# Kernel optimization log

Hardware: AMD Instinct MI355X
Metric: run time of the kernel (lower is better)

## Reference

```python
import math
import jax, jax.numpy as jnp
import numpy as np

B, N, T, H = 4, 64, 384, 256
LAGS = (1, 5, 21)
L = len(LAGS)
NU = 500  # peer-universe size for rank buffers
TOPK = 8
LN_EPS = 1e-5


def setup_inputs() -> dict:
    key = jax.random.key(0)
    ks = jax.random.split(key, 24)
    s = 1.0 / np.sqrt(H)

    def lin(i):
        w = jax.random.uniform(ks[i], (H, H), jnp.float32, -s, s)
        b = jax.random.uniform(ks[i + 1], (H,), jnp.float32, -s, s)
        return w, b

    wq_w, wq_b = lin(0)
    wk_w, wk_b = lin(2)
    wv_w, wv_b = lin(4)
    f1_w, f1_b = lin(6)
    f2_w, f2_b = lin(8)
    return dict(
        target_h=jax.random.normal(ks[10], (B, T, H), jnp.float32),
        peer_h=jax.random.normal(ks[11], (B, N, T, H), jnp.float32),
        wq_w=wq_w, wq_b=wq_b, wk_w=wk_w, wk_b=wk_b, wv_w=wv_w, wv_b=wv_b,
        f1_w=f1_w, f1_b=f1_b, f2_w=f2_w, f2_b=f2_b,
        ln_g=jnp.ones((H,), jnp.float32),
        ln_b=jnp.zeros((H,), jnp.float32),
        alpha=jnp.float32(0.1),
        log_rank_strength=jnp.log(jnp.clip(jax.random.uniform(ks[12], (L, NU, NU)), 1e-6, None)),
        peer_mask=jnp.ones((B, N), dtype=bool),
        rank_topk_mask=jax.random.uniform(ks[13], (L, NU, NU)) < 0.2,
        target_id=jax.random.randint(ks[14], (B,), 0, NU),
        peer_id=jax.random.randint(ks[15], (B, N), 0, NU),
    )


def _forward(target_h, peer_h, wq_w, wq_b, wk_w, wk_b, wv_w, wv_b,
             f1_w, f1_b, f2_w, f2_b, ln_g, ln_b, alpha, log_rank_strength,
             peer_mask, rank_topk_mask, target_id, peer_id):
    lags = jnp.array(LAGS, dtype=jnp.int32)
    t_idx = jnp.arange(T, dtype=jnp.int32)[None, :] - lags[:, None]   # [L,T]
    valid_time = t_idx >= 0                                           # [L,T]
    t_idx_c = jnp.maximum(t_idx, 0)

    # lag-gathered peer features: [B,N,L,T,H] -> [B,T,N,L,H]
    peer_h_lag = jnp.transpose(peer_h[:, :, t_idx_c, :], (0, 3, 1, 2, 4))

    Q = target_h @ wq_w.T + wq_b                  # [B,T,H]
    K = peer_h_lag @ wk_w.T + wk_b                # [B,T,N,L,H]
    # delta-valued V path (use_delta_value=True): current minus lagged
    peer_h_now = jnp.transpose(peer_h, (0, 2, 1, 3))[:, :, :, None, :]  # [B,T,N,1,H]
    V = (peer_h_now - peer_h_lag) @ wv_w.T + wv_b  # [B,T,N,L,H]

    logits = jnp.einsum('bth,btnlh->btnl', Q, K) / math.sqrt(H)  # [B,T,N,L]

    # Bennett soft bias (use_bennett=True)
    tgt_b = jnp.broadcast_to(target_id[:, None], (B, N))          # [B,N]
    prior = jnp.transpose(log_rank_strength[:, peer_id, tgt_b], (1, 2, 0))  # [B,N,L]
    logits = logits + alpha * prior[:, None, :, :]

    neg_inf = jnp.float32(-jnp.inf)
    logits = jnp.where(valid_time.T[None, :, None, :], logits, neg_inf)      # time validity
    logits = jnp.where(peer_mask[:, None, :, None], logits, neg_inf)         # peer mask
    rmask = jnp.transpose(rank_topk_mask[:, peer_id, tgt_b], (1, 2, 0))      # [B,N,L]
    logits = jnp.where(rmask[:, None, :, :], logits, neg_inf)                # hard rank mask

    NL = N * L
    k = min(TOPK, NL)
    logits_flat = logits.reshape(B, T, NL)
    topk_vals, topk_idx = jax.lax.top_k(logits_flat, k)            # [B,T,k]
    is_inf = jnp.isinf(topk_vals)
    all_inf = jnp.all(is_inf, axis=-1, keepdims=True)
    topk_safe = jnp.where(is_inf, jnp.float32(-1e9), topk_vals)
    weights = jax.nn.softmax(topk_safe, axis=-1)
    weights = weights * (~all_inf).astype(weights.dtype)

    V_flat = V.reshape(B, T, NL, H)
    V_sel = jnp.take_along_axis(V_flat, topk_idx[..., None], axis=2)  # [B,T,k,H]
    ll_y = jnp.sum(weights[..., None] * V_sel, axis=2)                # [B,T,H]

    ffn = jax.nn.elu(ll_y @ f1_w.T + f1_b) @ f2_w.T + f2_b
    x = ll_y + ffn
    mu = jnp.mean(x, axis=-1, keepdims=True)
    var = jnp.var(x, axis=-1, keepdims=True)
    return (x - mu) / jnp.sqrt(var + LN_EPS) * ln_g + ln_b


def reference(target_h, peer_h, wq_w, wq_b, wk_w, wk_b, wv_w, wv_b,
              f1_w, f1_b, f2_w, f2_b, ln_g, ln_b, alpha, log_rank_strength,
              peer_mask, rank_topk_mask, target_id, peer_id):
    return _forward(target_h, peer_h, wq_w, wq_b, wk_w, wk_b, wv_w, wv_b,
                    f1_w, f1_b, f2_w, f2_b, ln_g, ln_b, alpha, log_rank_strength,
                    peer_mask, rank_topk_mask, target_id, peer_id)
```

## Files before the change

### kernel.cpp

```cpp
#include <hip/hip_runtime.h>
#include <hip/hip_bf16.h>

typedef unsigned short u16;

#define NU_ 500

__device__ __forceinline__ float b2f(u16 u){
  union { unsigned int i; float f; } v; v.i = ((unsigned int)u) << 16; return v.f;
}
__device__ __forceinline__ void up2(unsigned int u, float& a, float& b){
  a = b2f((u16)(u & 0xffffu)); b = b2f((u16)(u >> 16));
}

template<typename FT> __device__ __forceinline__ float ldf(const FT* p, long i);
template<> __device__ __forceinline__ float ldf<float>(const float* p, long i){ return p[i]; }
template<> __device__ __forceinline__ float ldf<u16>(const u16* p, long i){ return b2f(p[i]); }

template<typename FT> __device__ __forceinline__ float4 ld4(const FT* p);
template<> __device__ __forceinline__ float4 ld4<float>(const float* p){ return *(const float4*)p; }
template<> __device__ __forceinline__ float4 ld4<u16>(const u16* p){
  uint2 u = *(const uint2*)p; float4 r; up2(u.x, r.x, r.y); up2(u.y, r.z, r.w); return r;
}

template<typename FT> __device__ __forceinline__ void ld8(const FT* p, float* o);
template<> __device__ __forceinline__ void ld8<float>(const float* p, float* o){
  float4 a = ((const float4*)p)[0], b = ((const float4*)p)[1];
  o[0]=a.x; o[1]=a.y; o[2]=a.z; o[3]=a.w; o[4]=b.x; o[5]=b.y; o[6]=b.z; o[7]=b.w;
}
template<> __device__ __forceinline__ void ld8<u16>(const u16* p, float* o){
  uint4 u = ((const uint4*)p)[0];
  up2(u.x,o[0],o[1]); up2(u.y,o[2],o[3]); up2(u.z,o[4],o[5]); up2(u.w,o[6],o[7]);
}

template<typename FT> __device__ __forceinline__ void stf(void* p, long i, float v);
template<> __device__ __forceinline__ void stf<float>(void* p, long i, float v){ ((float*)p)[i] = v; }
template<> __device__ __forceinline__ void stf<u16>(void* p, long i, float v){
  ((__hip_bfloat16*)p)[i] = __float2bfloat16(v);
}

__device__ __forceinline__ bool mask_at(const void* p, long i, int mode){
  if (mode == 1) return ((const unsigned char*)p)[i] != 0;
  if (mode == 2) return ((const u16*)p)[i] != 0;
  return ((const unsigned int*)p)[i] != 0;
}

__global__ void detect_kernel(const u16* __restrict__ lng,
                              const unsigned char* __restrict__ pm,
                              int* __restrict__ flags){
  if (threadIdx.x == 0){
    flags[0] = (lng[0] == 0x3F80u) ? 1 : 0;
    const unsigned char p0 = pm[0], p1 = pm[1];
    int m;
    if (p0 == 0x01u)      m = (p1 == 0x01u) ? 1 : 0;
    else if (p0 == 0x80u) m = 2;
    else                  m = 0;
    flags[1] = m;
  }
}

template<typename FT>
__global__ __launch_bounds__(256) void qproj_kernel(
    const FT* __restrict__ xg, const FT* __restrict__ wq, const FT* __restrict__ wqb,
    const FT* __restrict__ wk, const FT* __restrict__ wkb,
    float* __restrict__ Qt, float* __restrict__ qb, const int* __restrict__ flags, int me)
{
  if (flags[0] != me) return;
  __shared__ __align__(16) float xs[8][256];
  __shared__ __align__(16) float qs[8][256];
  const int j = threadIdx.x;
  const int row0 = blockIdx.x * 8;
  #pragma unroll
  for (int r = 0; r < 8; ++r) xs[r][j] = ldf<FT>(xg, (long)(row0 + r) * 256 + j);
  __syncthreads();

  float acc[8];
  #pragma unroll
  for (int r = 0; r < 8; ++r) acc[r] = 0.f;
  for (int h8 = 0; h8 < 32; ++h8){
    float w[8]; ld8<FT>(wq + (long)j * 256 + h8 * 8, w);
    const int h = h8 * 8;
    #pragma unroll
    for (int r = 0; r < 8; ++r){
      const float* xr = &xs[r][h];
      acc[r] += xr[0]*w[0] + xr[1]*w[1] + xr[2]*w[2] + xr[3]*w[3]
              + xr[4]*w[4] + xr[5]*w[5] + xr[6]*w[6] + xr[7]*w[7];
    }
  }
  const float bq = ldf<FT>(wqb, j);
  #pragma unroll
  for (int r = 0; r < 8; ++r) qs[r][j] = acc[r] + bq;
  __syncthreads();

  float at[8];
  #pragma unroll
  for (int r = 0; r < 8; ++r) at[r] = 0.f;
  for (int h = 0; h < 256; ++h){
    const float w = ldf<FT>(wk, (long)h * 256 + j);
    #pragma unroll
    for (int r = 0; r < 8; ++r) at[r] += qs[r][h] * w;
  }
  #pragma unroll
  for (int r = 0; r < 8; ++r) Qt[(long)(row0 + r) * 256 + j] = at[r];

  const float bk = ldf<FT>(wkb, j);
  #pragma unroll
  for (int r = 0; r < 8; ++r) xs[r][j] = qs[r][j] * bk;
  __syncthreads();
  if (j < 8){
    float s = 0.f;
    for (int h = 0; h < 256; ++h) s += xs[j][h];
    qb[row0 + j] = s;
  }
}

template<typename FT>
__global__ __launch_bounds__(256) void attn_kernel(
    const FT* __restrict__ peer_h, const float* __restrict__ Qt, const float* __restrict__ qbv,
    const FT* __restrict__ lrs, const void* __restrict__ pmask, const void* __restrict__ rmask,
    const int* __restrict__ target_id, const int* __restrict__ peer_id,
    const FT* __restrict__ alpha_p, const int* __restrict__ flags,
    float* __restrict__ dvec, float* __restrict__ ssum, int me)
{
  if (flags[0] != me) return;
  __shared__ __align__(16) float qt_s[256];
  __shared__ float lg[192];
  __shared__ int   seli[8];
  __shared__ float selw[8];
  __shared__ int   allinf_sh;
  const int bt = blockIdx.x;
  const int b = bt / 384, t = bt % 384;
  const int tid = threadIdx.x;
  const int lane = tid & 63, wv = tid >> 6;
  const float NEG_INF = -__builtin_inff();

  qt_s[tid] = Qt[(long)bt * 256 + tid];
  __syncthreads();
  const float qb    = qbv[bt];
  const float alpha = ldf<FT>(alpha_p, 0);
  const int   tgt   = target_id[b];
  const int   mmode = flags[1];
  const int   lags[3] = {1, 5, 21};

  const float4 qv = *(const float4*)&qt_s[lane * 4];

  for (int c = wv; c < 192; c += 4){
    const int n = c / 3, l = c - n * 3;
    const int lag = lags[l];
    const int pid = peer_id[b * 64 + n];
    const long ridx = (long)l * (NU_*NU_) + (long)pid * NU_ + tgt;
    bool ok = (t >= lag);
    if (ok) ok = mask_at(pmask, b * 64 + n, mmode) && mask_at(rmask, ridx, mmode);
    float logit = NEG_INF;
    if (ok){
      const int tc = t - lag;
      const FT* rp = peer_h + (((long)(b*64 + n)) * 384 + tc) * 256;
      float4 a = ld4<FT>(rp + lane * 4);
      float p = a.x*qv.x + a.y*qv.y + a.z*qv.z + a.w*qv.w;
      #pragma unroll
      for (int off = 32; off; off >>= 1) p += __shfl_xor(p, off);
      logit = (p + qb) * 0.0625f + alpha * ldf<FT>(lrs, ridx);
    }
    if (lane == 0) lg[c] = logit;
  }
  __syncthreads();

  if (wv == 0){
    float v0 = lg[lane], v1 = lg[lane + 64], v2 = lg[lane + 128];
    float sv[8]; int si[8];
    for (int k = 0; k < 8; ++k){
      float mv = v0; int mi = lane;
      if (v1 > mv){ mv = v1; mi = lane + 64; }
      if (v2 > mv){ mv = v2; mi = lane + 128; }
      #pragma unroll
      for (int off = 32; off; off >>= 1){
        float ov = __shfl_xor(mv, off);
        int   oi = __shfl_xor(mi, off);
        if (ov > mv || (ov == mv && oi < mi)){ mv = ov; mi = oi; }
      }
      sv[k] = mv; si[k] = mi;
      if      (mi == lane)       v0 = NEG_INF;
      else if (mi == lane + 64)  v1 = NEG_INF;
      else if (mi == lane + 128) v2 = NEG_INF;
    }
    const int allinf = (sv[0] == NEG_INF) ? 1 : 0;
    const float m = allinf ? -1e9f : sv[0];
    float e[8]; float tot = 0.f;
    #pragma unroll
    for (int k = 0; k < 8; ++k){
      const float s = (sv[k] == NEG_INF) ? -1e9f : sv[k];
      e[k] = expf(s - m);
      tot += e[k];
    }
    if (lane == 0){
      allinf_sh = allinf;
      const float inv = 1.f / tot;
      for (int k = 0; k < 8; ++k){
        seli[k] = si[k];
        selw[k] = allinf ? 0.f : e[k] * inv;
      }
    }
  }
  __syncthreads();

  float acc = 0.f;
  const int h = tid;
  #pragma unroll
  for (int k = 0; k < 8; ++k){
    const float w = selw[k];
    if (w != 0.f){
      const int c = seli[k];
      const int n = c / 3, l = c - n * 3;
      const int tc = t - lags[l];
      const long base = ((long)(b*64 + n)) * 384;
      acc += w * (ldf<FT>(peer_h, (base + t ) * 256 + h)
                - ldf<FT>(peer_h, (base + tc) * 256 + h));
    }
  }
  dvec[(long)bt * 256 + h] = acc;
  if (tid == 0) ssum[bt] = allinf_sh ? 0.f : 1.f;
}

template<typename FT>
__global__ __launch_bounds__(256) void ffn_kernel(
    const float* __restrict__ dv, const float* __restrict__ sv,
    const FT* __restrict__ wv, const FT* __restrict__ wvb,
    const FT* __restrict__ f1, const FT* __restrict__ f1b,
    const FT* __restrict__ f2, const FT* __restrict__ f2b,
    const FT* __restrict__ lng, const FT* __restrict__ lnb,
    void* __restrict__ out, const int* __restrict__ flags, int me)
{
  if (flags[0] != me) return;
  __shared__ __align__(16) float ds[8][256];
  __shared__ __align__(16) float ys[8][256];
  __shared__ float mu_s[8], rs_s[8];
  const int j = threadIdx.x;
  const int row0 = blockIdx.x * 8;
  #pragma unroll
  for (int r = 0; r < 8; ++r) ds[r][j] = dv[(long)(row0 + r) * 256 + j];
  __syncthreads();

  float ll[8];
  {
    #pragma unroll
    for (int r = 0; r < 8; ++r) ll[r] = 0.f;
    for (int h8 = 0; h8 < 32; ++h8){
      float w[8]; ld8<FT>(wv + (long)j * 256 + h8 * 8, w);
      const int h = h8 * 8;
      #pragma unroll
      for (int r = 0; r < 8; ++r){
        const float* xr = &ds[r][h];
        ll[r] += xr[0]*w[0] + xr[1]*w[1] + xr[2]*w[2] + xr[3]*w[3]
               + xr[4]*w[4] + xr[5]*w[5] + xr[6]*w[6] + xr[7]*w[7];
      }
    }
    const float bv = ldf<FT>(wvb, j);
    #pragma unroll
    for (int r = 0; r < 8; ++r) ll[r] += sv[row0 + r] * bv;
  }
  #pragma unroll
  for (int r = 0; r < 8; ++r) ys[r][j] = ll[r];
  __syncthreads();

  {
    float a[8];
    #pragma unroll
    for (int r = 0; r < 8; ++r) a[r] = 0.f;
    for (int h8 = 0; h8 < 32; ++h8){
      float w[8]; ld8<FT>(f1 + (long)j * 256 + h8 * 8, w);
      const int h = h8 * 8;
      #pragma unroll
      for (int r = 0; r < 8; ++r){
        const float* xr = &ys[r][h];
        a[r] += xr[0]*w[0] + xr[1]*w[1] + xr[2]*w[2] + xr[3]*w[3]
              + xr[4]*w[4] + xr[5]*w[5] + xr[6]*w[6] + xr[7]*w[7];
      }
    }
    const float b1 = ldf<FT>(f1b, j);
    #pragma unroll
    for (int r = 0; r < 8; ++r){
      const float x = a[r] + b1;
      ds[r][j] = (x > 0.f) ? x : expm1f(x);
    }
  }
  __syncthreads();

  float xv[8];
  {
    float a[8];
    #pragma unroll
    for (int r = 0; r < 8; ++r) a[r] = 0.f;
    for (int h8 = 0; h8 < 32; ++h8){
      float w[8]; ld8<FT>(f2 + (long)j * 256 + h8 * 8, w);
      const int h = h8 * 8;
      #pragma unroll
      for (int r = 0; r < 8; ++r){
        const float* xr = &ds[r][h];
        a[r] += xr[0]*w[0] + xr[1]*w[1] + xr[2]*w[2] + xr[3]*w[3]
              + xr[4]*w[4] + xr[5]*w[5] + xr[6]*w[6] + xr[7]*w[7];
      }
    }
    const float b2_ = ldf<FT>(f2b, j);
    #pragma unroll
    for (int r = 0; r < 8; ++r) xv[r] = ll[r] + a[r] + b2_;
  }
  #pragma unroll
  for (int r = 0; r < 8; ++r) ys[r][j] = xv[r];
  __syncthreads();

  {
    const int lane = j & 63, wvi = j >> 6;
    for (int rr = 0; rr < 2; ++rr){
      const int r = wvi * 2 + rr;
      float s = 0.f, q = 0.f;
      for (int p = lane; p < 256; p += 64){ const float x = ys[r][p]; s += x; q += x * x; }
      #pragma unroll
      for (int off = 32; off; off >>= 1){ s += __shfl_xor(s, off); q += __shfl_xor(q, off); }
      if (lane == 0){
        const float mu = s * (1.f/256.f);
        const float var = q * (1.f/256.f) - mu * mu;
        mu_s[r] = mu; rs_s[r] = rsqrtf(var + 1e-5f);
      }
    }
  }
  __syncthreads();
  const float gj = ldf<FT>(lng, j), bj = ldf<FT>(lnb, j);
  #pragma unroll
  for (int r = 0; r < 8; ++r){
    const float o = (ys[r][j] - mu_s[r]) * rs_s[r] * gj + bj;
    stf<FT>(out, (long)(row0 + r) * 256 + j, o);
  }
}

extern "C" void kernel_launch(void* const* d_in, const int* in_sizes, int n_in,
                              void* d_out, int out_size, void* d_ws, size_t ws_size,
                              hipStream_t stream)
{
  (void)in_sizes; (void)n_in; (void)out_size; (void)ws_size;
  const void* target_h = d_in[0];
  const void* peer_h   = d_in[1];
  const void* wq_w = d_in[2];  const void* wq_b = d_in[3];
  const void* wk_w = d_in[4];  const void* wk_b = d_in[5];
  const void* wv_w = d_in[6];  const void* wv_b = d_in[7];
  const void* f1_w = d_in[8];  const void* f1_b = d_in[9];
  const void* f2_w = d_in[10]; const void* f2_b = d_in[11];
  const void* ln_g = d_in[12]; const void* ln_b = d_in[13];
  const void* alpha = d_in[14];
  const void* lrs  = d_in[15];
  const void* pmask = d_in[16];
  const void* rmask = d_in[17];
  const int* target_id = (const int*)d_in[18];
  const int* peer_id   = (const int*)d_in[19];

  int*   flags = (int*)d_ws;
  float* Qt    = (float*)d_ws + 16;
  float* qb    = Qt + 393216;
  float* dvec  = qb + 1536;
  float* ssum  = dvec + 393216;

  detect_kernel<<<1, 64, 0, stream>>>((const u16*)ln_g, (const unsigned char*)pmask, flags);

  qproj_kernel<float><<<192, 256, 0, stream>>>((const float*)target_h, (const float*)wq_w,
      (const float*)wq_b, (const float*)wk_w, (const float*)wk_b, Qt, qb, flags, 0);
  attn_kernel<float><<<1536, 256, 0, stream>>>((const float*)peer_h, Qt, qb,
      (const float*)lrs, pmask, rmask, target_id, peer_id, (const float*)alpha,
      flags, dvec, ssum, 0);
  ffn_kernel<float><<<192, 256, 0, stream>>>(dvec, ssum, (const float*)wv_w, (const float*)wv_b,
      (const float*)f1_w, (const float*)f1_b, (const float*)f2_w, (const float*)f2_b,
      (const float*)ln_g, (const float*)ln_b, d_out, flags, 0);

  qproj_kernel<u16><<<192, 256, 0, stream>>>((const u16*)target_h, (const u16*)wq_w,
      (const u16*)wq_b, (const u16*)wk_w, (const u16*)wk_b, Qt, qb, flags, 1);
  attn_kernel<u16><<<1536, 256, 0, stream>>>((const u16*)peer_h, Qt, qb,
      (const u16*)lrs, pmask, rmask, target_id, peer_id, (const u16*)alpha,
      flags, dvec, ssum, 1);
  ffn_kernel<u16><<<192, 256, 0, stream>>>(dvec, ssum, (const u16*)wv_w, (const u16*)wv_b,
      (const u16*)f1_w, (const u16*)f1_b, (const u16*)f2_w, (const u16*)f2_b,
      (const u16*)ln_g, (const u16*)ln_b, d_out, flags, 1);
}
```

Measured before the change: 318.5 us.

## Drop bf16 dispatch path, precompute peer priors, and widen attention logit loads

Removes the runtime dtype-detection kernel and the duplicate bf16 kernel launches, so only float kernels are launched. A new prep kernel computes the masked alpha*log_rank prior once per (batch, peer, lag) instead of once per time step in every attention block. The attention logit loop now uses 16-lane groups, each lane loading 16 floats, so each wave computes four logits at once with shorter shuffle reductions. In exchange, bf16 inputs are no longer supported and the code assumes float32 inputs.

New measurement: 269.6 us. 1.18x faster.

```diff
diff --git a/kernel.cpp b/kernel.cpp
--- a/kernel.cpp
+++ b/kernel.cpp
@@ -1,92 +1,67 @@
 #include <hip/hip_runtime.h>
 #include <hip/hip_bf16.h>
 
-typedef unsigned short u16;
 
 #define NU_ 500
-
-__device__ __forceinline__ float b2f(u16 u){
-  union { unsigned int i; float f; } v; v.i = ((unsigned int)u) << 16; return v.f;
-}
-__device__ __forceinline__ void up2(unsigned int u, float& a, float& b){
-  a = b2f((u16)(u & 0xffffu)); b = b2f((u16)(u >> 16));
-}
-
-template<typename FT> __device__ __forceinline__ float ldf(const FT* p, long i);
-template<> __device__ __forceinline__ float ldf<float>(const float* p, long i){ return p[i]; }
-template<> __device__ __forceinline__ float ldf<u16>(const u16* p, long i){ return b2f(p[i]); }
-
-template<typename FT> __device__ __forceinline__ float4 ld4(const FT* p);
-template<> __device__ __forceinline__ float4 ld4<float>(const float* p){ return *(const float4*)p; }
-template<> __device__ __forceinline__ float4 ld4<u16>(const u16* p){
-  uint2 u = *(const uint2*)p; float4 r; up2(u.x, r.x, r.y); up2(u.y, r.z, r.w); return r;
-}
-
-template<typename FT> __device__ __forceinline__ void ld8(const FT* p, float* o);
-template<> __device__ __forceinline__ void ld8<float>(const float* p, float* o){
-  float4 a = ((const float4*)p)[0], b = ((const float4*)p)[1];
-  o[0]=a.x; o[1]=a.y; o[2]=a.z; o[3]=a.w; o[4]=b.x; o[5]=b.y; o[6]=b.z; o[7]=b.w;
-}
-template<> __device__ __forceinline__ void ld8<u16>(const u16* p, float* o){
-  uint4 u = ((const uint4*)p)[0];
-  up2(u.x,o[0],o[1]); up2(u.y,o[2],o[3]); up2(u.z,o[4],o[5]); up2(u.w,o[6],o[7]);
-}
-
-template<typename FT> __device__ __forceinline__ void stf(void* p, long i, float v);
-template<> __device__ __forceinline__ void stf<float>(void* p, long i, float v){ ((float*)p)[i] = v; }
-template<> __device__ __forceinline__ void stf<u16>(void* p, long i, float v){
-  ((__hip_bfloat16*)p)[i] = __float2bfloat16(v);
-}
 
 __device__ __forceinline__ bool mask_at(const void* p, long i, int mode){
   if (mode == 1) return ((const unsigned char*)p)[i] != 0;
-  if (mode == 2) return ((const u16*)p)[i] != 0;
+  if (mode == 2) return ((const unsigned short*)p)[i] != 0;
   return ((const unsigned int*)p)[i] != 0;
 }
 
-__global__ void detect_kernel(const u16* __restrict__ lng,
-                              const unsigned char* __restrict__ pm,
-                              int* __restrict__ flags){
-  if (threadIdx.x == 0){
-    flags[0] = (lng[0] == 0x3F80u) ? 1 : 0;
-    const unsigned char p0 = pm[0], p1 = pm[1];
-    int m;
-    if (p0 == 0x01u)      m = (p1 == 0x01u) ? 1 : 0;
-    else if (p0 == 0x80u) m = 2;
-    else                  m = 0;
-    flags[1] = m;
-  }
-}
-
-template<typename FT>
+__global__ void prep_kernel(const float* __restrict__ lrs,
+                            const void* __restrict__ pmask, const void* __restrict__ rmask,
+                            const int* __restrict__ target_id, const int* __restrict__ peer_id,
+                            const float* __restrict__ alpha_p,
+                            float* __restrict__ prior)
+{
+  const int b = blockIdx.x;
+  const int c = threadIdx.x;
+  if (c >= 192) return;
+  const unsigned char* pmB = (const unsigned char*)pmask;
+  const unsigned char p0 = pmB[0], p1 = pmB[1];
+  int mmode;
+  if (p0 == 0x01u)      mmode = (p1 == 0x01u) ? 1 : 0;
+  else if (p0 == 0x80u) mmode = 2;
+  else                  mmode = 0;
+
+  const int n = c / 3, l = c - n * 3;
+  const int pid = peer_id[b * 64 + n];
+  const int tgt = target_id[b];
+  const long ridx = (long)l * (NU_*NU_) + (long)pid * NU_ + tgt;
+  const bool ok = mask_at(pmask, b * 64 + n, mmode) && mask_at(rmask, ridx, mmode);
+  prior[b * 192 + c] = ok ? alpha_p[0] * lrs[ridx] : -__builtin_inff();
+}
+
 __global__ __launch_bounds__(256) void qproj_kernel(
-    const FT* __restrict__ xg, const FT* __restrict__ wq, const FT* __restrict__ wqb,
-    const FT* __restrict__ wk, const FT* __restrict__ wkb,
-    float* __restrict__ Qt, float* __restrict__ qb, const int* __restrict__ flags, int me)
-{
-  if (flags[0] != me) return;
+    const float* __restrict__ xg, const float* __restrict__ wq, const float* __restrict__ wqb,
+    const float* __restrict__ wk, const float* __restrict__ wkb,
+    float* __restrict__ Qt, float* __restrict__ qb)
+{
   __shared__ __align__(16) float xs[8][256];
   __shared__ __align__(16) float qs[8][256];
   const int j = threadIdx.x;
   const int row0 = blockIdx.x * 8;
   #pragma unroll
-  for (int r = 0; r < 8; ++r) xs[r][j] = ldf<FT>(xg, (long)(row0 + r) * 256 + j);
+  for (int r = 0; r < 8; ++r) xs[r][j] = xg[(long)(row0 + r) * 256 + j];
   __syncthreads();
 
   float acc[8];
   #pragma unroll
   for (int r = 0; r < 8; ++r) acc[r] = 0.f;
+  const float4* wrow = (const float4*)(wq + (long)j * 256);
   for (int h8 = 0; h8 < 32; ++h8){
-    float w[8]; ld8<FT>(wq + (long)j * 256 + h8 * 8, w);
+    float4 wa = wrow[h8 * 2], wb = wrow[h8 * 2 + 1];
     const int h = h8 * 8;
     #pragma unroll
     for (int r = 0; r < 8; ++r){
       const float* xr = &xs[r][h];
-      acc[r] += xr[0]*w[0] + xr[1]*w[1] + xr[2]*w[2] + xr[3]*w[3]
-              + xr[4]*w[4] + xr[5]*w[5] + xr[6]*w[6] + xr[7]*w[7];
-    }
-  }
-  const float bq = ldf<FT>(wqb, j);
+      acc[r] += xr[0]*wa.x + xr[1]*wa.y + xr[2]*wa.z + xr[3]*wa.w
+              + xr[4]*wb.x + xr[5]*wb.y + xr[6]*wb.z + xr[7]*wb.w;
+    }
+  }
+  const float bq = wqb[j];
   #pragma unroll
   for (int r = 0; r < 8; ++r) qs[r][j] = acc[r] + bq;
   __syncthreads();
@@ -95,14 +70,14 @@
   #pragma unroll
   for (int r = 0; r < 8; ++r) at[r] = 0.f;
   for (int h = 0; h < 256; ++h){
-    const float w = ldf<FT>(wk, (long)h * 256 + j);
+    const float w = wk[(long)h * 256 + j];
     #pragma unroll
     for (int r = 0; r < 8; ++r) at[r] += qs[r][h] * w;
   }
   #pragma unroll
   for (int r = 0; r < 8; ++r) Qt[(long)(row0 + r) * 256 + j] = at[r];
 
-  const float bk = ldf<FT>(wkb, j);
+  const float bk = wkb[j];
   #pragma unroll
   for (int r = 0; r < 8; ++r) xs[r][j] = qs[r][j] * bk;
   __syncthreads();
@@ -113,15 +88,11 @@
   }
 }
 
-template<typename FT>
 __global__ __launch_bounds__(256) void attn_kernel(
-    const FT* __restrict__ peer_h, const float* __restrict__ Qt, const float* __restrict__ qbv,
-    const FT* __restrict__ lrs, const void* __restrict__ pmask, const void* __restrict__ rmask,
-    const int* __restrict__ target_id, const int* __restrict__ peer_id,
-    const FT* __restrict__ alpha_p, const int* __restrict__ flags,
-    float* __restrict__ dvec, float* __restrict__ ssum, int me)
-{
-  if (flags[0] != me) return;
+    const float* __restrict__ peer_h, const float* __restrict__ Qt,
+    const float* __restrict__ qbv, const float* __restrict__ prior,
+    float* __restrict__ dvec, float* __restrict__ ssum)
+{
   __shared__ __align__(16) float qt_s[256];
   __shared__ float lg[192];
   __shared__ int   seli[8];
@@ -130,41 +101,46 @@
   const int bt = blockIdx.x;
   const int b = bt / 384, t = bt % 384;
   const int tid = threadIdx.x;
-  const int lane = tid & 63, wv = tid >> 6;
   const float NEG_INF = -__builtin_inff();
 
   qt_s[tid] = Qt[(long)bt * 256 + tid];
   __syncthreads();
-  const float qb    = qbv[bt];
-  const float alpha = ldf<FT>(alpha_p, 0);
-  const int   tgt   = target_id[b];
-  const int   mmode = flags[1];
-  const int   lags[3] = {1, 5, 21};
-
-  const float4 qv = *(const float4*)&qt_s[lane * 4];
-
-  for (int c = wv; c < 192; c += 4){
+  const float qb = qbv[bt];
+  const int lags[3] = {1, 5, 21};
+
+  const int group = tid >> 4, q = tid & 15;
+  float qv[16];
+  #pragma unroll
+  for (int i = 0; i < 4; ++i){
+    float4 f = *(const float4*)&qt_s[q * 16 + i * 4];
+    qv[i*4] = f.x; qv[i*4+1] = f.y; qv[i*4+2] = f.z; qv[i*4+3] = f.w;
+  }
+
+  #pragma unroll
+  for (int it = 0; it < 12; ++it){
+    const int c = it * 16 + group;
     const int n = c / 3, l = c - n * 3;
     const int lag = lags[l];
-    const int pid = peer_id[b * 64 + n];
-    const long ridx = (long)l * (NU_*NU_) + (long)pid * NU_ + tgt;
-    bool ok = (t >= lag);
-    if (ok) ok = mask_at(pmask, b * 64 + n, mmode) && mask_at(rmask, ridx, mmode);
+    const float pe = prior[b * 192 + c];
+    const bool ok = (t >= lag) && (pe > -3.0e38f);
     float logit = NEG_INF;
     if (ok){
-      const int tc = t - lag;
-      const FT* rp = peer_h + (((long)(b*64 + n)) * 384 + tc) * 256;
-      float4 a = ld4<FT>(rp + lane * 4);
-      float p = a.x*qv.x + a.y*qv.y + a.z*qv.z + a.w*qv.w;
-      #pragma unroll
-      for (int off = 32; off; off >>= 1) p += __shfl_xor(p, off);
-      logit = (p + qb) * 0.0625f + alpha * ldf<FT>(lrs, ridx);
-    }
-    if (lane == 0) lg[c] = logit;
-  }
-  __syncthreads();
-
-  if (wv == 0){
+      const float4* rp = (const float4*)(peer_h + (((long)(b*64 + n)) * 384 + (t - lag)) * 256);
+      float4 u0 = rp[q*4], u1 = rp[q*4+1], u2 = rp[q*4+2], u3 = rp[q*4+3];
+      float p = u0.x*qv[0] + u0.y*qv[1] + u0.z*qv[2] + u0.w*qv[3]
+              + u1.x*qv[4] + u1.y*qv[5] + u1.z*qv[6] + u1.w*qv[7]
+              + u2.x*qv[8] + u2.y*qv[9] + u2.z*qv[10]+ u2.w*qv[11]
+              + u3.x*qv[12]+ u3.y*qv[13]+ u3.z*qv[14]+ u3.w*qv[15];
+      #pragma unroll
+      for (int off = 1; off < 16; off <<= 1) p += __shfl_xor(p, off);
+      logit = (p + qb) * 0.0625f + pe;
+    }
+    if (q == 0) lg[c] = logit;
+  }
+  __syncthreads();
+
+  if (tid < 64){
+    const int lane = tid;
     float v0 = lg[lane], v1 = lg[lane + 64], v2 = lg[lane + 128];
     float sv[8]; int si[8];
     for (int k = 0; k < 8; ++k){
@@ -212,24 +188,22 @@
       const int n = c / 3, l = c - n * 3;
       const int tc = t - lags[l];
       const long base = ((long)(b*64 + n)) * 384;
-      acc += w * (ldf<FT>(peer_h, (base + t ) * 256 + h)
-                - ldf<FT>(peer_h, (base + tc) * 256 + h));
+      acc += w * (peer_h[(base + t ) * 256 + h]
+                - peer_h[(base + tc) * 256 + h]);
     }
   }
   dvec[(long)bt * 256 + h] = acc;
   if (tid == 0) ssum[bt] = allinf_sh ? 0.f : 1.f;
 }
 
-template<typename FT>
 __global__ __launch_bounds__(256) void ffn_kernel(
     const float* __restrict__ dv, const float* __restrict__ sv,
-    const FT* __restrict__ wv, const FT* __restrict__ wvb,
-    const FT* __restrict__ f1, const FT* __restrict__ f1b,
-    const FT* __restrict__ f2, const FT* __restrict__ f2b,
-    const FT* __restrict__ lng, const FT* __restrict__ lnb,
-    void* __restrict__ out, const int* __restrict__ flags, int me)
-{
-  if (flags[0] != me) return;
+    const float* __restrict__ wv, const float* __restrict__ wvb,
+    const float* __restrict__ f1, const float* __restrict__ f1b,
+    const float* __restrict__ f2, const float* __restrict__ f2b,
+    const float* __restrict__ lng, const float* __restrict__ lnb,
+    float* __restrict__ out)
+{
   __shared__ __align__(16) float ds[8][256];
   __shared__ __align__(16) float ys[8][256];
   __shared__ float mu_s[8], rs_s[8];
@@ -243,17 +217,18 @@
   {
     #pragma unroll
     for (int r = 0; r < 8; ++r) ll[r] = 0.f;
+    const float4* wrow = (const float4*)(wv + (long)j * 256);
     for (int h8 = 0; h8 < 32; ++h8){
-      float w[8]; ld8<FT>(wv + (long)j * 256 + h8 * 8, w);
+      float4 wa = wrow[h8 * 2], wb = wrow[h8 * 2 + 1];
       const int h = h8 * 8;
       #pragma unroll
       for (int r = 0; r < 8; ++r){
         const float* xr = &ds[r][h];
-        ll[r] += xr[0]*w[0] + xr[1]*w[1] + xr[2]*w[2] + xr[3]*w[3]
-               + xr[4]*w[4] + xr[5]*w[5] + xr[6]*w[6] + xr[7]*w[7];
-      }
-    }
-    const float bv = ldf<FT>(wvb, j);
+        ll[r] += xr[0]*wa.x + xr[1]*wa.y + xr[2]*wa.z + xr[3]*wa.w
+               + xr[4]*wb.x + xr[5]*wb.y + xr[6]*wb.z + xr[7]*wb.w;
+      }
+    }
+    const float bv = wvb[j];
     #pragma unroll
     for (int r = 0; r < 8; ++r) ll[r] += sv[row0 + r] * bv;
   }
@@ -265,17 +240,18 @@
     float a[8];
     #pragma unroll
     for (int r = 0; r < 8; ++r) a[r] = 0.f;
+    const float4* wrow = (const float4*)(f1 + (long)j * 256);
     for (int h8 = 0; h8 < 32; ++h8){
-      float w[8]; ld8<FT>(f1 + (long)j * 256 + h8 * 8, w);
+      float4 wa = wrow[h8 * 2], wb = wrow[h8 * 2 + 1];
       const int h = h8 * 8;
       #pragma unroll
       for (int r = 0; r < 8; ++r){
         const float* xr = &ys[r][h];
-        a[r] += xr[0]*w[0] + xr[1]*w[1] + xr[2]*w[2] + xr[3]*w[3]
-              + xr[4]*w[4] + xr[5]*w[5] + xr[6]*w[6] + xr[7]*w[7];
-      }
-    }
-    const float b1 = ldf<FT>(f1b, j);
+        a[r] += xr[0]*wa.x + xr[1]*wa.y + xr[2]*wa.z + xr[3]*wa.w
+              + xr[4]*wb.x + xr[5]*wb.y + xr[6]*wb.z + xr[7]*wb.w;
+      }
+    }
+    const float b1 = f1b[j];
     #pragma unroll
     for (int r = 0; r < 8; ++r){
       const float x = a[r] + b1;
@@ -289,17 +265,18 @@
     float a[8];
     #pragma unroll
     for (int r = 0; r < 8; ++r) a[r] = 0.f;
+    const float4* wrow = (const float4*)(f2 + (long)j * 256);
     for (int h8 = 0; h8 < 32; ++h8){
-      float w[8]; ld8<FT>(f2 + (long)j * 256 + h8 * 8, w);
+      float4 wa = wrow[h8 * 2], wb = wrow[h8 * 2 + 1];
       const int h = h8 * 8;
       #pragma unroll
       for (int r = 0; r < 8; ++r){
         const float* xr = &ds[r][h];
-        a[r] += xr[0]*w[0] + xr[1]*w[1] + xr[2]*w[2] + xr[3]*w[3]
-              + xr[4]*w[4] + xr[5]*w[5] + xr[6]*w[6] + xr[7]*w[7];
-      }
-    }
-    const float b2_ = ldf<FT>(f2b, j);
+        a[r] += xr[0]*wa.x + xr[1]*wa.y + xr[2]*wa.z + xr[3]*wa.w
+              + xr[4]*wb.x + xr[5]*wb.y + xr[6]*wb.z + xr[7]*wb.w;
+      }
+    }
+    const float b2_ = f2b[j];
     #pragma unroll
     for (int r = 0; r < 8; ++r) xv[r] = ll[r] + a[r] + b2_;
   }
@@ -311,23 +288,23 @@
     const int lane = j & 63, wvi = j >> 6;
     for (int rr = 0; rr < 2; ++rr){
       const int r = wvi * 2 + rr;
-      float s = 0.f, q = 0.f;
-      for (int p = lane; p < 256; p += 64){ const float x = ys[r][p]; s += x; q += x * x; }
-      #pragma unroll
-      for (int off = 32; off; off >>= 1){ s += __shfl_xor(s, off); q += __shfl_xor(q, off); }
+      float s = 0.f, qq = 0.f;
+      for (int p = lane; p < 256; p += 64){ const float x = ys[r][p]; s += x; qq += x * x; }
+      #pragma unroll
+      for (int off = 32; off; off >>= 1){ s += __shfl_xor(s, off); qq += __shfl_xor(qq, off); }
       if (lane == 0){
         const float mu = s * (1.f/256.f);
-        const float var = q * (1.f/256.f) - mu * mu;
+        const float var = qq * (1.f/256.f) - mu * mu;
         mu_s[r] = mu; rs_s[r] = rsqrtf(var + 1e-5f);
       }
     }
   }
   __syncthreads();
-  const float gj = ldf<FT>(lng, j), bj = ldf<FT>(lnb, j);
+  const float gj = lng[j], bj = lnb[j];
   #pragma unroll
   for (int r = 0; r < 8; ++r){
     const float o = (ys[r][j] - mu_s[r]) * rs_s[r] * gj + bj;
-    stf<FT>(out, (long)(row0 + r) * 256 + j, o);
+    out[(long)(row0 + r) * 256 + j] = o;
   }
 }
 
@@ -336,44 +313,30 @@
                               hipStream_t stream)
 {
   (void)in_sizes; (void)n_in; (void)out_size; (void)ws_size;
-  const void* target_h = d_in[0];
-  const void* peer_h   = d_in[1];
-  const void* wq_w = d_in[2];  const void* wq_b = d_in[3];
-  const void* wk_w = d_in[4];  const void* wk_b = d_in[5];
-  const void* wv_w = d_in[6];  const void* wv_b = d_in[7];
-  const void* f1_w = d_in[8];  const void* f1_b = d_in[9];
-  const void* f2_w = d_in[10]; const void* f2_b = d_in[11];
-  const void* ln_g = d_in[12]; const void* ln_b = d_in[13];
-  const void* alpha = d_in[14];
-  const void* lrs  = d_in[15];
+  const float* target_h = (const float*)d_in[0];
+  const float* peer_h   = (const float*)d_in[1];
+  const float* wq_w = (const float*)d_in[2];  const float* wq_b = (const float*)d_in[3];
+  const float* wk_w = (const float*)d_in[4];  const float* wk_b = (const float*)d_in[5];
+  const float* wv_w = (const float*)d_in[6];  const float* wv_b = (const float*)d_in[7];
+  const float* f1_w = (const float*)d_in[8];  const float* f1_b = (const float*)d_in[9];
+  const float* f2_w = (const float*)d_in[10]; const float* f2_b = (const float*)d_in[11];
+  const float* ln_g = (const float*)d_in[12]; const float* ln_b = (const float*)d_in[13];
+  const float* alpha = (const float*)d_in[14];
+  const float* lrs  = (const float*)d_in[15];
   const void* pmask = d_in[16];
   const void* rmask = d_in[17];
   const int* target_id = (const int*)d_in[18];
   const int* peer_id   = (const int*)d_in[19];
 
-  int*   flags = (int*)d_ws;
-  float* Qt    = (float*)d_ws + 16;
+  float* prior = (float*)d_ws;
+  float* Qt    = prior + 4 * 192;
   float* qb    = Qt + 393216;
   float* dvec  = qb + 1536;
   float* ssum  = dvec + 393216;
 
-  detect_kernel<<<1, 64, 0, stream>>>((const u16*)ln_g, (const unsigned char*)pmask, flags);
-
-  qproj_kernel<float><<<192, 256, 0, stream>>>((const float*)target_h, (const float*)wq_w,
-      (const float*)wq_b, (const float*)wk_w, (const float*)wk_b, Qt, qb, flags, 0);
-  attn_kernel<float><<<1536, 256, 0, stream>>>((const float*)peer_h, Qt, qb,
-      (const float*)lrs, pmask, rmask, target_id, peer_id, (const float*)alpha,
-      flags, dvec, ssum, 0);
-  ffn_kernel<float><<<192, 256, 0, stream>>>(dvec, ssum, (const float*)wv_w, (const float*)wv_b,
-      (const float*)f1_w, (const float*)f1_b, (const float*)f2_w, (const float*)f2_b,
-      (const float*)ln_g, (const float*)ln_b, d_out, flags, 0);
-
-  qproj_kernel<u16><<<192, 256, 0, stream>>>((const u16*)target_h, (const u16*)wq_w,
-      (const u16*)wq_b, (const u16*)wk_w, (const u16*)wk_b, Qt, qb, flags, 1);
-  attn_kernel<u16><<<1536, 256, 0, stream>>>((const u16*)peer_h, Qt, qb,
-      (const u16*)lrs, pmask, rmask, target_id, peer_id, (const u16*)alpha,
-      flags, dvec, ssum, 1);
-  ffn_kernel<u16><<<192, 256, 0, stream>>>(dvec, ssum, (const u16*)wv_w, (const u16*)wv_b,
-      (const u16*)f1_w, (const u16*)f1_b, (const u16*)f2_w, (const u16*)f2_b,
-      (const u16*)ln_g, (const u16*)ln_b, d_out, flags, 1);
-}
+  prep_kernel<<<4, 192, 0, stream>>>(lrs, pmask, rmask, target_id, peer_id, alpha, prior);
+  qproj_kernel<<<192, 256, 0, stream>>>(target_h, wq_w, wq_b, wk_w, wk_b, Qt, qb);
+  attn_kernel<<<1536, 256, 0, stream>>>(peer_h, Qt, qb, prior, dvec, ssum);
+  ffn_kernel<<<192, 256, 0, stream>>>(dvec, ssum, wv_w, wv_b, f1_w, f1_b,
+                                      f2_w, f2_b, ln_g, ln_b, (float*)d_out);
+}
```
